# Optimization experiments

Hardware: AMD Instinct MI355X
Metric: run time of the kernel (lower is better)

## Reference

```python
import jax, jax.numpy as jnp
import numpy as np

EMBED_DIM = 512
HEAD_SIZE = 32
HEAD_DIM = 32  # constant used for scaling in the original code
B, T = 4, 4096


def setup_inputs() -> dict:
    key = jax.random.key(0)
    ks = jax.random.split(key, 9)
    s = 0.02
    return {
        "x": jax.random.normal(ks[0], (B, T, EMBED_DIM), dtype=jnp.float32),
        "Wq": jax.random.normal(ks[1], (EMBED_DIM, HEAD_SIZE), dtype=jnp.float32) * s,
        "bq": jnp.zeros((HEAD_SIZE,), dtype=jnp.float32),
        "Wk": jax.random.normal(ks[2], (EMBED_DIM, HEAD_SIZE), dtype=jnp.float32) * s,
        "bk": jnp.zeros((HEAD_SIZE,), dtype=jnp.float32),
        "Wv": jax.random.normal(ks[3], (EMBED_DIM, HEAD_SIZE), dtype=jnp.float32) * s,
        "bv": jnp.zeros((HEAD_SIZE,), dtype=jnp.float32),
        "Wp": jax.random.normal(ks[4], (HEAD_SIZE, EMBED_DIM), dtype=jnp.float32) * s,
        "bp": jnp.zeros((EMBED_DIM,), dtype=jnp.float32),
    }


def reference(x, Wq, bq, Wk, bk, Wv, bv, Wp, bp):
    # q, k, v: [B, T, head_size]
    q = x @ Wq + bq
    k = x @ Wk + bk
    v = x @ Wv + bv
    # scores: [B, T, T]
    scores = jnp.einsum("btd,bsd->bts", q, k) / jnp.sqrt(jnp.float32(HEAD_DIM))
    t = x.shape[1]
    causal = jnp.tril(jnp.ones((t, t), dtype=bool))  # lower-triangular incl. diag
    scores = jnp.where(causal, scores, jnp.float32(-1e9))
    weights = jax.nn.softmax(scores, axis=-1)
    attn = jnp.einsum("bts,bsd->btd", weights, v)  # [B, T, head_size]
    return attn @ Wp + bp  # [B, T, embed_dim]
```

## Files before the change

kernel.cpp:

```cpp
#include <hip/hip_runtime.h>
#include <hip/hip_bf16.h>

#define TSEQ   4096
#define NB     4
#define EMB    512
#define HS     32
#define NQ     16384

typedef float  f32x4  __attribute__((ext_vector_type(4)));
typedef __bf16 bf16x8 __attribute__((ext_vector_type(8)));
typedef __bf16 bf16x4 __attribute__((ext_vector_type(4)));

__global__ __launch_bounds__(256) void qkv_mfma(
    const float* __restrict__ x,
    const float* __restrict__ Wq, const float* __restrict__ bq,
    const float* __restrict__ Wk, const float* __restrict__ bk,
    const float* __restrict__ Wv, const float* __restrict__ bv,
    __bf16* __restrict__ qbf, __bf16* __restrict__ kbf, __bf16* __restrict__ vtb)
{
    const int tid  = threadIdx.x;
    const int lane = tid & 63;
    const int w    = tid >> 6;
    const int lr = lane & 15;
    const int lh = lane >> 4;
    const int tok0 = blockIdx.x * 16;
    const int k0   = w * 128;

    const float qs = 0.17677669529663687f;
    const float* xp = x + (size_t)(tok0 + lr) * EMB + k0 + lh * 8;

    const float* wbase[6] = { Wq + lr, Wq + 16 + lr,
                              Wk + lr, Wk + 16 + lr,
                              Wv + lr, Wv + 16 + lr };

    auto ldfrag = [&](int f, int koff) -> bf16x8 {
        const float* p = wbase[f] + (size_t)(k0 + koff + lh * 8) * HS;
        const float s = (f < 2) ? qs : 1.0f;
        bf16x8 r;
        #pragma unroll
        for (int j = 0; j < 8; ++j)
            r[j] = (__bf16)(p[(size_t)j * HS] * s);
        return r;
    };
    auto ldx = [&](int koff) -> bf16x8 {
        const float4 a4 = *(const float4*)(xp + koff);
        const float4 b4 = *(const float4*)(xp + koff + 4);
        return bf16x8{ (__bf16)a4.x, (__bf16)a4.y, (__bf16)a4.z, (__bf16)a4.w,
                       (__bf16)b4.x, (__bf16)b4.y, (__bf16)b4.z, (__bf16)b4.w };
    };

    const f32x4 z = {0.f, 0.f, 0.f, 0.f};
    f32x4 acc[6] = {z, z, z, z, z, z};

    bf16x8 xf_c, wf_c[6], xf_n, wf_n[6];
    xf_c = ldx(0);
    #pragma unroll
    for (int f = 0; f < 6; ++f) wf_c[f] = ldfrag(f, 0);

    #pragma unroll
    for (int kt = 0; kt < 128; kt += 32) {
        const int ktn = (kt + 32 < 128) ? (kt + 32) : kt;
        xf_n = ldx(ktn);
        #pragma unroll
        for (int f = 0; f < 6; ++f) wf_n[f] = ldfrag(f, ktn);

        acc[0] = __builtin_amdgcn_mfma_f32_16x16x32_bf16(wf_c[0], xf_c, acc[0], 0, 0, 0);
        acc[1] = __builtin_amdgcn_mfma_f32_16x16x32_bf16(wf_c[1], xf_c, acc[1], 0, 0, 0);
        acc[2] = __builtin_amdgcn_mfma_f32_16x16x32_bf16(wf_c[2], xf_c, acc[2], 0, 0, 0);
        acc[3] = __builtin_amdgcn_mfma_f32_16x16x32_bf16(wf_c[3], xf_c, acc[3], 0, 0, 0);
        acc[4] = __builtin_amdgcn_mfma_f32_16x16x32_bf16(xf_c, wf_c[4], acc[4], 0, 0, 0);
        acc[5] = __builtin_amdgcn_mfma_f32_16x16x32_bf16(xf_c, wf_c[5], acc[5], 0, 0, 0);

        xf_c = xf_n;
        #pragma unroll
        for (int f = 0; f < 6; ++f) wf_c[f] = wf_n[f];
    }

    __shared__ float red[3 * 6 * 256];
    if (w > 0) {
        #pragma unroll
        for (int i = 0; i < 6; ++i)
            *(f32x4*)&red[((w - 1) * 6 + i) * 256 + lane * 4] = acc[i];
    }
    __syncthreads();
    if (w != 0) return;

    #pragma unroll
    for (int i = 0; i < 6; ++i)
        #pragma unroll
        for (int ww = 0; ww < 3; ++ww)
            acc[i] += *(const f32x4*)&red[(ww * 6 + i) * 256 + lane * 4];

    #pragma unroll
    for (int f = 0; f < 2; ++f) {
        const int cb = f * 16 + lh * 4;
        const float4 bq4 = *(const float4*)(bq + cb);
        const float4 bk4 = *(const float4*)(bk + cb);
        bf16x4 oq = { (__bf16)(acc[f][0] + bq4.x * qs), (__bf16)(acc[f][1] + bq4.y * qs),
                      (__bf16)(acc[f][2] + bq4.z * qs), (__bf16)(acc[f][3] + bq4.w * qs) };
        bf16x4 ok = { (__bf16)(acc[2+f][0] + bk4.x), (__bf16)(acc[2+f][1] + bk4.y),
                      (__bf16)(acc[2+f][2] + bk4.z), (__bf16)(acc[2+f][3] + bk4.w) };
        *(bf16x4*)(qbf + (size_t)(tok0 + lr) * HS + cb) = oq;
        *(bf16x4*)(kbf + (size_t)(tok0 + lr) * HS + cb) = ok;
    }
    {
        const int b    = tok0 >> 12;
        const int t_in = (tok0 & (TSEQ - 1)) + lh * 4;
        #pragma unroll
        for (int f = 0; f < 2; ++f) {
            const int d = f * 16 + lr;
            const float bv1 = bv[d];
            bf16x4 o = { (__bf16)(acc[4+f][0] + bv1), (__bf16)(acc[4+f][1] + bv1),
                         (__bf16)(acc[4+f][2] + bv1), (__bf16)(acc[4+f][3] + bv1) };
            *(bf16x4*)(vtb + ((size_t)(b * HS + d)) * TSEQ + t_in) = o;
        }
    }
}

__device__ __forceinline__ void s_stage2(
    const bf16x8 ck0, const bf16x8 ck1,
    const bf16x8 qb0, const bf16x8 qb1,
    int kt, int q0, int lr, int lh, int swz,
    float lp[2], char* Pb)
{
    const f32x4 z = {0.f, 0.f, 0.f, 0.f};
    f32x4 st00 = __builtin_amdgcn_mfma_f32_16x16x32_bf16(ck0, qb0, z, 0, 0, 0);
    f32x4 st01 = __builtin_amdgcn_mfma_f32_16x16x32_bf16(ck1, qb0, z, 0, 0, 0);
    f32x4 st10 = __builtin_amdgcn_mfma_f32_16x16x32_bf16(ck0, qb1, z, 0, 0, 0);
    f32x4 st11 = __builtin_amdgcn_mfma_f32_16x16x32_bf16(ck1, qb1, z, 0, 0, 0);

    float P[2][2][4];
    #pragma unroll
    for (int r = 0; r < 4; ++r) {
        P[0][0][r] = st00[r]; P[0][1][r] = st01[r];
        P[1][0][r] = st10[r]; P[1][1][r] = st11[r];
    }

    if (kt != q0) {
        #pragma unroll
        for (int qh = 0; qh < 2; ++qh)
            #pragma unroll
            for (int kh = 0; kh < 2; ++kh)
                #pragma unroll
                for (int r = 0; r < 4; ++r)
                    P[qh][kh][r] = __expf(P[qh][kh][r]);
    } else {
        #pragma unroll
        for (int qh = 0; qh < 2; ++qh)
            #pragma unroll
            for (int kh = 0; kh < 2; ++kh)
                #pragma unroll
                for (int r = 0; r < 4; ++r) {
                    const int key_l = kh * 16 + lh * 4 + r;
                    const int q_l   = qh * 16 + lr;
                    P[qh][kh][r] = (key_l <= q_l) ? __expf(P[qh][kh][r]) : 0.f;
                }
    }

    #pragma unroll
    for (int qh = 0; qh < 2; ++qh)
        #pragma unroll
        for (int kh = 0; kh < 2; ++kh)
            #pragma unroll
            for (int r = 0; r < 4; ++r)
                lp[qh] += P[qh][kh][r];

    #pragma unroll
    for (int qh = 0; qh < 2; ++qh)
        #pragma unroll
        for (int kh = 0; kh < 2; ++kh) {
            const int q    = qh * 16 + lr;
            const int byte = q * 128 + ((kh * 32 + lh * 8) ^ swz);
            bf16x4 pk = { (__bf16)P[qh][kh][0], (__bf16)P[qh][kh][1],
                          (__bf16)P[qh][kh][2], (__bf16)P[qh][kh][3] };
            *(bf16x4*)(Pb + byte) = pk;
        }
}

__device__ __forceinline__ void strip_proc2(
    int kt0, int kend, int q0,
    const bf16x8 qb0, const bf16x8 qb1,
    const __bf16* kbase, const __bf16* vbase,
    char* Pl,
    f32x4 o[4], float lp[2],
    int lr, int lh, int swz, int rdA, int rdB)
{
    if (kt0 >= kend) return;

    bf16x8 kf0 = *(const bf16x8*)(kbase + (size_t)kt0 * HS);
    bf16x8 kf1 = *(const bf16x8*)(kbase + (size_t)(kt0 + 16) * HS);
    bf16x8 vf0 = *(const bf16x8*)(vbase + kt0);
    bf16x8 vf1 = *(const bf16x8*)(vbase + kt0 + 16 * TSEQ);

    bf16x8 cv0p, cv1p;
    int pb = 1;
    {
        const bf16x8 ck0 = kf0, ck1 = kf1;
        cv0p = vf0; cv1p = vf1;
        const int ktn = (kt0 + 256 < kend) ? (kt0 + 256) : kt0;
        kf0 = *(const bf16x8*)(kbase + (size_t)ktn * HS);
        kf1 = *(const bf16x8*)(kbase + (size_t)(ktn + 16) * HS);
        vf0 = *(const bf16x8*)(vbase + ktn);
        vf1 = *(const bf16x8*)(vbase + ktn + 16 * TSEQ);
        s_stage2(ck0, ck1, qb0, qb1, kt0, q0, lr, lh, swz, lp, Pl);
    }

    for (int kt = kt0 + 256; kt < kend; kt += 256) {
        const bf16x8 ck0 = kf0, ck1 = kf1, cv0 = vf0, cv1 = vf1;
        const int ktn = (kt + 256 < kend) ? (kt + 256) : kt;
        kf0 = *(const bf16x8*)(kbase + (size_t)ktn * HS);
        kf1 = *(const bf16x8*)(kbase + (size_t)(ktn + 16) * HS);
        vf0 = *(const bf16x8*)(vbase + ktn);
        vf1 = *(const bf16x8*)(vbase + ktn + 16 * TSEQ);

        const char* pbase = Pl + (pb ^ 1) * 4096;
        const bf16x8 pa0 = *(const bf16x8*)(pbase + rdA);
        const bf16x8 pa1 = *(const bf16x8*)(pbase + rdB);

        s_stage2(ck0, ck1, qb0, qb1, kt, q0, lr, lh, swz, lp, Pl + pb * 4096);

        o[0] = __builtin_amdgcn_mfma_f32_16x16x32_bf16(pa0, cv0p, o[0], 0, 0, 0);
        o[1] = __builtin_amdgcn_mfma_f32_16x16x32_bf16(pa0, cv1p, o[1], 0, 0, 0);
        o[2] = __builtin_amdgcn_mfma_f32_16x16x32_bf16(pa1, cv0p, o[2], 0, 0, 0);
        o[3] = __builtin_amdgcn_mfma_f32_16x16x32_bf16(pa1, cv1p, o[3], 0, 0, 0);

        cv0p = cv0; cv1p = cv1; pb ^= 1;
    }

    {
        const char* pbase = Pl + (pb ^ 1) * 4096;
        const bf16x8 pa0 = *(const bf16x8*)(pbase + rdA);
        const bf16x8 pa1 = *(const bf16x8*)(pbase + rdB);
        o[0] = __builtin_amdgcn_mfma_f32_16x16x32_bf16(pa0, cv0p, o[0], 0, 0, 0);
        o[1] = __builtin_amdgcn_mfma_f32_16x16x32_bf16(pa0, cv1p, o[1], 0, 0, 0);
        o[2] = __builtin_amdgcn_mfma_f32_16x16x32_bf16(pa1, cv0p, o[2], 0, 0, 0);
        o[3] = __builtin_amdgcn_mfma_f32_16x16x32_bf16(pa1, cv1p, o[3], 0, 0, 0);
    }
}

__global__ __launch_bounds__(512) void attn_fused(
    const __bf16* __restrict__ qbf, const __bf16* __restrict__ kbf,
    const __bf16* __restrict__ vtb,
    const float* __restrict__ Wp, const float* __restrict__ bp,
    float* __restrict__ out)
{
    const int p   = blockIdx.x;
    const int b   = blockIdx.y;
    const int tid = threadIdx.x;
    const int w    = tid >> 6;
    const int lane = tid & 63;
    const int lr = lane & 15;
    const int lh = lane >> 4;

    const int n0  = p + 1;
    const int q00 = p * 32;
    const int q01 = (127 - p) * 32;

    extern __shared__ char smem[];
    char*   myPl   = smem + w * 8192;
    float*  red    = (float*)smem;
    float*  lpred  = (float*)(smem + 65536);
    __bf16* attn_s = (__bf16*)(smem + 65536 + 2048);

    const __bf16* qp0 = qbf + ((size_t)(b * TSEQ + q00 + lr)) * HS + lh * 8;
    const __bf16* qp1 = qbf + ((size_t)(b * TSEQ + q01 + lr)) * HS + lh * 8;
    const bf16x8 qb0s0 = *(const bf16x8*)qp0;
    const bf16x8 qb1s0 = *(const bf16x8*)(qp0 + 16 * HS);
    const bf16x8 qb0s1 = *(const bf16x8*)qp1;
    const bf16x8 qb1s1 = *(const bf16x8*)(qp1 + 16 * HS);

    const __bf16* kbase = kbf + ((size_t)(b * TSEQ + lr)) * HS + lh * 8;
    const __bf16* vbase = vtb + (size_t)(b * HS + lr) * TSEQ + lh * 8;

    const int swz = (lr & 7) << 4;
    const int rdA = lr * 128 + ((lh * 16) ^ swz);
    const int rdB = (16 + lr) * 128 + ((lh * 16) ^ swz);

    const f32x4 z = {0.f, 0.f, 0.f, 0.f};
    f32x4 o0[4] = {z, z, z, z};
    f32x4 o1[4] = {z, z, z, z};
    float lp0[2] = {0.f, 0.f}, lp1[2] = {0.f, 0.f};

    strip_proc2(w * 32, q00 + 32, q00, qb0s0, qb1s0, kbase, vbase, myPl,
                o0, lp0, lr, lh, swz, rdA, rdB);
    const int tb = n0 + ((w - n0) & 7);
    strip_proc2((tb - n0) * 32, q01 + 32, q01, qb0s1, qb1s1, kbase, vbase, myPl,
                o1, lp1, lr, lh, swz, rdA, rdB);

    #pragma unroll
    for (int qh = 0; qh < 2; ++qh) {
        lp0[qh] += __shfl_xor(lp0[qh], 16, 64);
        lp0[qh] += __shfl_xor(lp0[qh], 32, 64);
        lp1[qh] += __shfl_xor(lp1[qh], 16, 64);
        lp1[qh] += __shfl_xor(lp1[qh], 32, 64);
    }

    __syncthreads();

    #pragma unroll
    for (int f = 0; f < 4; ++f) {
        *(f32x4*)&red[((w * 2 + 0) * 4 + f) * 256 + lane * 4] = o0[f];
        *(f32x4*)&red[((w * 2 + 1) * 4 + f) * 256 + lane * 4] = o1[f];
    }
    if (lh == 0) {
        #pragma unroll
        for (int qh = 0; qh < 2; ++qh) {
            lpred[(w * 2 + 0) * 32 + qh * 16 + lr] = lp0[qh];
            lpred[(w * 2 + 1) * 32 + qh * 16 + lr] = lp1[qh];
        }
    }
    __syncthreads();

    {
        const int s  = w >> 2;
        const int f  = w & 3;
        const int qh = f >> 1;
        const int dh = f & 1;
        f32x4 sum = z;
        #pragma unroll
        for (int ww = 0; ww < 8; ++ww)
            sum += *(const f32x4*)&red[((ww * 2 + s) * 4 + f) * 256 + lane * 4];

        #pragma unroll
        for (int r = 0; r < 4; ++r) {
            const int q = qh * 16 + lh * 4 + r;
            float L = 0.f;
            #pragma unroll
            for (int ww = 0; ww < 8; ++ww)
                L += lpred[(ww * 2 + s) * 32 + q];
            attn_s[(s * 32 + q) * 32 + dh * 16 + lr] = (__bf16)(sum[r] / L);
        }
    }
    __syncthreads();

    {
        const int sp = w >> 2;
        const int c0 = (w & 3) * 128;
        const int qb0i = (sp == 0) ? q00 : q01;
        const __bf16* as = attn_s + sp * 1024;
        const bf16x8 a0 = *(const bf16x8*)(as + lr * 32 + lh * 8);
        const bf16x8 a1 = *(const bf16x8*)(as + (16 + lr) * 32 + lh * 8);

        #pragma unroll
        for (int g = 0; g < 8; ++g) {
            const int c = c0 + g * 16;
            const float* wsrc = Wp + (size_t)(lh * 8) * EMB + c + lr;
            bf16x8 wa;
            #pragma unroll
            for (int j = 0; j < 8; ++j)
                wa[j] = (__bf16)wsrc[(size_t)j * EMB];

            f32x4 d0 = __builtin_amdgcn_mfma_f32_16x16x32_bf16(wa, a0, z, 0, 0, 0);
            f32x4 d1 = __builtin_amdgcn_mfma_f32_16x16x32_bf16(wa, a1, z, 0, 0, 0);

            const float4 b4 = *(const float4*)(bp + c + lh * 4);
            const float4 ov0 = make_float4(d0[0] + b4.x, d0[1] + b4.y,
                                           d0[2] + b4.z, d0[3] + b4.w);
            const float4 ov1 = make_float4(d1[0] + b4.x, d1[1] + b4.y,
                                           d1[2] + b4.z, d1[3] + b4.w);
            *(float4*)(out + (size_t)(b * TSEQ + qb0i + lr)      * EMB + c + lh * 4) = ov0;
            *(float4*)(out + (size_t)(b * TSEQ + qb0i + 16 + lr) * EMB + c + lh * 4) = ov1;
        }
    }
}

extern "C" void kernel_launch(void* const* d_in, const int* in_sizes, int n_in,
                              void* d_out, int out_size, void* d_ws, size_t ws_size,
                              hipStream_t stream)
{
    const float* x  = (const float*)d_in[0];
    const float* Wq = (const float*)d_in[1];
    const float* bq = (const float*)d_in[2];
    const float* Wk = (const float*)d_in[3];
    const float* bk = (const float*)d_in[4];
    const float* Wv = (const float*)d_in[5];
    const float* bv = (const float*)d_in[6];
    const float* Wp = (const float*)d_in[7];
    const float* bp = (const float*)d_in[8];
    float* out = (float*)d_out;

    char* ws = (char*)d_ws;
    __bf16* qbf = (__bf16*)(ws);
    __bf16* kbf = (__bf16*)(ws + (size_t)1 * 1024 * 1024);
    __bf16* vtb = (__bf16*)(ws + (size_t)2 * 1024 * 1024);

    qkv_mfma<<<dim3(NQ / 16), 256, 0, stream>>>(x, Wq, bq, Wk, bk, Wv, bv,
                                                qbf, kbf, vtb);
    attn_fused<<<dim3(64, NB), 512, 71680, stream>>>(qbf, kbf, vtb, Wp, bp, out);
}
```

Before: 43.33 us.

## Fuse QKV projection and attention into one cooperative kernel with grid sync

Merges the QKV projection kernel into the attention kernel as a single cooperative launch of 256 blocks. Each block projects 64 tokens with 8 waves that split the K dimension and reduce partial sums through shared memory, then the whole grid synchronizes before the attention phase. This removes a kernel launch and the gap between the two kernels. In exchange, the projection runs on only 256 blocks instead of 1024, and it adds the cost of a grid-wide barrier.

```diff
diff --git a/kernel.cpp b/kernel.cpp
--- a/kernel.cpp
+++ b/kernel.cpp
@@ -1,5 +1,8 @@
 #include <hip/hip_runtime.h>
 #include <hip/hip_bf16.h>
+#include <hip/hip_cooperative_groups.h>
+
+namespace cg = cooperative_groups;
 
 #define TSEQ   4096
 #define NB     4
@@ -11,111 +14,6 @@
 typedef __bf16 bf16x8 __attribute__((ext_vector_type(8)));
 typedef __bf16 bf16x4 __attribute__((ext_vector_type(4)));
 
-__global__ __launch_bounds__(256) void qkv_mfma(
-    const float* __restrict__ x,
-    const float* __restrict__ Wq, const float* __restrict__ bq,
-    const float* __restrict__ Wk, const float* __restrict__ bk,
-    const float* __restrict__ Wv, const float* __restrict__ bv,
-    __bf16* __restrict__ qbf, __bf16* __restrict__ kbf, __bf16* __restrict__ vtb)
-{
-    const int tid  = threadIdx.x;
-    const int lane = tid & 63;
-    const int w    = tid >> 6;
-    const int lr = lane & 15;
-    const int lh = lane >> 4;
-    const int tok0 = blockIdx.x * 16;
-    const int k0   = w * 128;
-
-    const float qs = 0.17677669529663687f;
-    const float* xp = x + (size_t)(tok0 + lr) * EMB + k0 + lh * 8;
-
-    const float* wbase[6] = { Wq + lr, Wq + 16 + lr,
-                              Wk + lr, Wk + 16 + lr,
-                              Wv + lr, Wv + 16 + lr };
-
-    auto ldfrag = [&](int f, int koff) -> bf16x8 {
-        const float* p = wbase[f] + (size_t)(k0 + koff + lh * 8) * HS;
-        const float s = (f < 2) ? qs : 1.0f;
-        bf16x8 r;
-        #pragma unroll
-        for (int j = 0; j < 8; ++j)
-            r[j] = (__bf16)(p[(size_t)j * HS] * s);
-        return r;
-    };
-    auto ldx = [&](int koff) -> bf16x8 {
-        const float4 a4 = *(const float4*)(xp + koff);
-        const float4 b4 = *(const float4*)(xp + koff + 4);
-        return bf16x8{ (__bf16)a4.x, (__bf16)a4.y, (__bf16)a4.z, (__bf16)a4.w,
-                       (__bf16)b4.x, (__bf16)b4.y, (__bf16)b4.z, (__bf16)b4.w };
-    };
-
-    const f32x4 z = {0.f, 0.f, 0.f, 0.f};
-    f32x4 acc[6] = {z, z, z, z, z, z};
-
-    bf16x8 xf_c, wf_c[6], xf_n, wf_n[6];
-    xf_c = ldx(0);
-    #pragma unroll
-    for (int f = 0; f < 6; ++f) wf_c[f] = ldfrag(f, 0);
-
-    #pragma unroll
-    for (int kt = 0; kt < 128; kt += 32) {
-        const int ktn = (kt + 32 < 128) ? (kt + 32) : kt;
-        xf_n = ldx(ktn);
-        #pragma unroll
-        for (int f = 0; f < 6; ++f) wf_n[f] = ldfrag(f, ktn);
-
-        acc[0] = __builtin_amdgcn_mfma_f32_16x16x32_bf16(wf_c[0], xf_c, acc[0], 0, 0, 0);
-        acc[1] = __builtin_amdgcn_mfma_f32_16x16x32_bf16(wf_c[1], xf_c, acc[1], 0, 0, 0);
-        acc[2] = __builtin_amdgcn_mfma_f32_16x16x32_bf16(wf_c[2], xf_c, acc[2], 0, 0, 0);
-        acc[3] = __builtin_amdgcn_mfma_f32_16x16x32_bf16(wf_c[3], xf_c, acc[3], 0, 0, 0);
-        acc[4] = __builtin_amdgcn_mfma_f32_16x16x32_bf16(xf_c, wf_c[4], acc[4], 0, 0, 0);
-        acc[5] = __builtin_amdgcn_mfma_f32_16x16x32_bf16(xf_c, wf_c[5], acc[5], 0, 0, 0);
-
-        xf_c = xf_n;
-        #pragma unroll
-        for (int f = 0; f < 6; ++f) wf_c[f] = wf_n[f];
-    }
-
-    __shared__ float red[3 * 6 * 256];
-    if (w > 0) {
-        #pragma unroll
-        for (int i = 0; i < 6; ++i)
-            *(f32x4*)&red[((w - 1) * 6 + i) * 256 + lane * 4] = acc[i];
-    }
-    __syncthreads();
-    if (w != 0) return;
-
-    #pragma unroll
-    for (int i = 0; i < 6; ++i)
-        #pragma unroll
-        for (int ww = 0; ww < 3; ++ww)
-            acc[i] += *(const f32x4*)&red[(ww * 6 + i) * 256 + lane * 4];
-
-    #pragma unroll
-    for (int f = 0; f < 2; ++f) {
-        const int cb = f * 16 + lh * 4;
-        const float4 bq4 = *(const float4*)(bq + cb);
-        const float4 bk4 = *(const float4*)(bk + cb);
-        bf16x4 oq = { (__bf16)(acc[f][0] + bq4.x * qs), (__bf16)(acc[f][1] + bq4.y * qs),
-                      (__bf16)(acc[f][2] + bq4.z * qs), (__bf16)(acc[f][3] + bq4.w * qs) };
-        bf16x4 ok = { (__bf16)(acc[2+f][0] + bk4.x), (__bf16)(acc[2+f][1] + bk4.y),
-                      (__bf16)(acc[2+f][2] + bk4.z), (__bf16)(acc[2+f][3] + bk4.w) };
-        *(bf16x4*)(qbf + (size_t)(tok0 + lr) * HS + cb) = oq;
-        *(bf16x4*)(kbf + (size_t)(tok0 + lr) * HS + cb) = ok;
-    }
-    {
-        const int b    = tok0 >> 12;
-        const int t_in = (tok0 & (TSEQ - 1)) + lh * 4;
-        #pragma unroll
-        for (int f = 0; f < 2; ++f) {
-            const int d = f * 16 + lr;
-            const float bv1 = bv[d];
-            bf16x4 o = { (__bf16)(acc[4+f][0] + bv1), (__bf16)(acc[4+f][1] + bv1),
-                         (__bf16)(acc[4+f][2] + bv1), (__bf16)(acc[4+f][3] + bv1) };
-            *(bf16x4*)(vtb + ((size_t)(b * HS + d)) * TSEQ + t_in) = o;
-        }
-    }
-}
 
 __device__ __forceinline__ void s_stage2(
     const bf16x8 ck0, const bf16x8 ck1,
@@ -238,25 +136,118 @@
     }
 }
 
-__global__ __launch_bounds__(512) void attn_fused(
-    const __bf16* __restrict__ qbf, const __bf16* __restrict__ kbf,
-    const __bf16* __restrict__ vtb,
+__global__ __launch_bounds__(512) void fused_all(
+    const float* __restrict__ x,
+    const float* __restrict__ Wq, const float* __restrict__ bq,
+    const float* __restrict__ Wk, const float* __restrict__ bk,
+    const float* __restrict__ Wv, const float* __restrict__ bv,
     const float* __restrict__ Wp, const float* __restrict__ bp,
+    __bf16* __restrict__ qbf, __bf16* __restrict__ kbf, __bf16* __restrict__ vtb,
     float* __restrict__ out)
 {
-    const int p   = blockIdx.x;
-    const int b   = blockIdx.y;
-    const int tid = threadIdx.x;
+    extern __shared__ char smem[];
+    const int bid  = blockIdx.x;
+    const int tid  = threadIdx.x;
     const int w    = tid >> 6;
     const int lane = tid & 63;
     const int lr = lane & 15;
     const int lh = lane >> 4;
+    const f32x4 z = {0.f, 0.f, 0.f, 0.f};
+    const float qs = 0.17677669529663687f;
+
+    {
+        float* red = (float*)smem;
+        const int k0 = w * 64;
+        const float* wsel[6] = { Wq, Wq, Wk, Wk, Wv, Wv };
+
+        bf16x8 wf[6][2];
+        #pragma unroll
+        for (int f = 0; f < 6; ++f) {
+            const float s = (f < 2) ? qs : 1.0f;
+            const int cc = (f & 1) * 16 + lr;
+            #pragma unroll
+            for (int kk = 0; kk < 2; ++kk) {
+                const float* pp = wsel[f] + (size_t)(k0 + kk * 32 + lh * 8) * HS + cc;
+                #pragma unroll
+                for (int j = 0; j < 8; ++j)
+                    wf[f][kk][j] = (__bf16)(pp[(size_t)j * HS] * s);
+            }
+        }
+
+        #pragma unroll 1
+        for (int g = 0; g < 4; ++g) {
+            const int tok0 = bid * 64 + g * 16;
+            const float* xp = x + (size_t)(tok0 + lr) * EMB + k0 + lh * 8;
+            const float4 a0 = *(const float4*)(xp);
+            const float4 b0 = *(const float4*)(xp + 4);
+            const float4 a1 = *(const float4*)(xp + 32);
+            const float4 b1 = *(const float4*)(xp + 36);
+            const bf16x8 xf0 = bf16x8{ (__bf16)a0.x, (__bf16)a0.y, (__bf16)a0.z, (__bf16)a0.w,
+                                       (__bf16)b0.x, (__bf16)b0.y, (__bf16)b0.z, (__bf16)b0.w };
+            const bf16x8 xf1 = bf16x8{ (__bf16)a1.x, (__bf16)a1.y, (__bf16)a1.z, (__bf16)a1.w,
+                                       (__bf16)b1.x, (__bf16)b1.y, (__bf16)b1.z, (__bf16)b1.w };
+
+            f32x4 acc[6] = {z, z, z, z, z, z};
+            acc[0] = __builtin_amdgcn_mfma_f32_16x16x32_bf16(wf[0][0], xf0, acc[0], 0, 0, 0);
+            acc[1] = __builtin_amdgcn_mfma_f32_16x16x32_bf16(wf[1][0], xf0, acc[1], 0, 0, 0);
+            acc[2] = __builtin_amdgcn_mfma_f32_16x16x32_bf16(wf[2][0], xf0, acc[2], 0, 0, 0);
+            acc[3] = __builtin_amdgcn_mfma_f32_16x16x32_bf16(wf[3][0], xf0, acc[3], 0, 0, 0);
+            acc[4] = __builtin_amdgcn_mfma_f32_16x16x32_bf16(xf0, wf[4][0], acc[4], 0, 0, 0);
+            acc[5] = __builtin_amdgcn_mfma_f32_16x16x32_bf16(xf0, wf[5][0], acc[5], 0, 0, 0);
+            acc[0] = __builtin_amdgcn_mfma_f32_16x16x32_bf16(wf[0][1], xf1, acc[0], 0, 0, 0);
+            acc[1] = __builtin_amdgcn_mfma_f32_16x16x32_bf16(wf[1][1], xf1, acc[1], 0, 0, 0);
+            acc[2] = __builtin_amdgcn_mfma_f32_16x16x32_bf16(wf[2][1], xf1, acc[2], 0, 0, 0);
+            acc[3] = __builtin_amdgcn_mfma_f32_16x16x32_bf16(wf[3][1], xf1, acc[3], 0, 0, 0);
+            acc[4] = __builtin_amdgcn_mfma_f32_16x16x32_bf16(xf1, wf[4][1], acc[4], 0, 0, 0);
+            acc[5] = __builtin_amdgcn_mfma_f32_16x16x32_bf16(xf1, wf[5][1], acc[5], 0, 0, 0);
+
+            #pragma unroll
+            for (int i = 0; i < 6; ++i)
+                *(f32x4*)&red[(w * 6 + i) * 256 + lane * 4] = acc[i];
+            __syncthreads();
+
+            if (w < 6) {
+                f32x4 sum = z;
+                #pragma unroll
+                for (int ww = 0; ww < 8; ++ww)
+                    sum += *(const f32x4*)&red[(ww * 6 + w) * 256 + lane * 4];
+
+                if (w < 2) {
+                    const int cb = w * 16 + lh * 4;
+                    const float4 b4 = *(const float4*)(bq + cb);
+                    bf16x4 o4 = { (__bf16)(sum[0] + b4.x * qs), (__bf16)(sum[1] + b4.y * qs),
+                                  (__bf16)(sum[2] + b4.z * qs), (__bf16)(sum[3] + b4.w * qs) };
+                    *(bf16x4*)(qbf + (size_t)(tok0 + lr) * HS + cb) = o4;
+                } else if (w < 4) {
+                    const int cb = (w - 2) * 16 + lh * 4;
+                    const float4 b4 = *(const float4*)(bk + cb);
+                    bf16x4 o4 = { (__bf16)(sum[0] + b4.x), (__bf16)(sum[1] + b4.y),
+                                  (__bf16)(sum[2] + b4.z), (__bf16)(sum[3] + b4.w) };
+                    *(bf16x4*)(kbf + (size_t)(tok0 + lr) * HS + cb) = o4;
+                } else {
+                    const int f    = w - 4;
+                    const int b    = tok0 >> 12;
+                    const int t_in = (tok0 & (TSEQ - 1)) + lh * 4;
+                    const int d    = f * 16 + lr;
+                    const float bv1 = bv[d];
+                    bf16x4 o4 = { (__bf16)(sum[0] + bv1), (__bf16)(sum[1] + bv1),
+                                  (__bf16)(sum[2] + bv1), (__bf16)(sum[3] + bv1) };
+                    *(bf16x4*)(vtb + ((size_t)(b * HS + d)) * TSEQ + t_in) = o4;
+                }
+            }
+            __syncthreads();
+        }
+    }
+
+    cg::this_grid().sync();
+
+    const int p = bid & 63;
+    const int b = bid >> 6;
 
     const int n0  = p + 1;
     const int q00 = p * 32;
     const int q01 = (127 - p) * 32;
 
-    extern __shared__ char smem[];
     char*   myPl   = smem + w * 8192;
     float*  red    = (float*)smem;
     float*  lpred  = (float*)(smem + 65536);
@@ -276,7 +267,6 @@
     const int rdA = lr * 128 + ((lh * 16) ^ swz);
     const int rdB = (16 + lr) * 128 + ((lh * 16) ^ swz);
 
-    const f32x4 z = {0.f, 0.f, 0.f, 0.f};
     f32x4 o0[4] = {z, z, z, z};
     f32x4 o1[4] = {z, z, z, z};
     float lp0[2] = {0.f, 0.f}, lp1[2] = {0.f, 0.f};
@@ -384,7 +374,9 @@
     __bf16* kbf = (__bf16*)(ws + (size_t)1 * 1024 * 1024);
     __bf16* vtb = (__bf16*)(ws + (size_t)2 * 1024 * 1024);
 
-    qkv_mfma<<<dim3(NQ / 16), 256, 0, stream>>>(x, Wq, bq, Wk, bk, Wv, bv,
-                                                qbf, kbf, vtb);
-    attn_fused<<<dim3(64, NB), 512, 71680, stream>>>(qbf, kbf, vtb, Wp, bp, out);
+    void* args[] = { (void*)&x, (void*)&Wq, (void*)&bq, (void*)&Wk, (void*)&bk,
+                     (void*)&Wv, (void*)&bv, (void*)&Wp, (void*)&bp,
+                     (void*)&qbf, (void*)&kbf, (void*)&vtb, (void*)&out };
+    hipLaunchCooperativeKernel((const void*)fused_all, dim3(256), dim3(512),
+                               args, 71680, stream);
 }
```

Result: slower. 77.05 us (+77.8%).
